# Optimization experiments

Hardware: AMD Instinct MI355X
Metric: run time of the kernel (lower is better)

The kernel has to match this reference:

```python
import jax, jax.numpy as jnp
import numpy as np

N, E, D_IN, D_HID, D_OUT = 100000, 1200000, 64, 64, 32


def setup_inputs() -> dict:
    key = jax.random.key(0)
    ks = jax.random.split(key, 8)
    x = jax.random.normal(ks[0], (N, D_IN), dtype=jnp.float32)
    edge_index = jax.random.randint(ks[1], (2, E), 0, N, dtype=jnp.int64)

    def w(k, din, dout):
        return jax.random.normal(k, (din, dout), dtype=jnp.float32) / jnp.sqrt(jnp.float32(din))

    return {
        "x": x,
        "edge_index": edge_index,
        # SAGEConv layer 1: lin_l (on aggregated neighbors, with bias) + lin_r (on self, no bias)
        "W_l1": w(ks[2], D_IN, D_HID),
        "W_r1": w(ks[3], D_IN, D_HID),
        "b1": jnp.zeros((D_HID,), jnp.float32),
        # SAGEConv layer 2
        "W_l2": w(ks[4], D_HID, D_OUT),
        "W_r2": w(ks[5], D_HID, D_OUT),
        "b2": jnp.zeros((D_OUT,), jnp.float32),
    }


def _sage_conv(x, src, dst, W_l, W_r, b, n_nodes):
    # mean-aggregate source features into destination nodes (PyG default 'mean')
    summed = jax.ops.segment_sum(x[src], dst, num_segments=n_nodes)          # [N, D]
    deg = jax.ops.segment_sum(jnp.ones(src.shape, x.dtype), dst, num_segments=n_nodes)
    mean = summed / jnp.maximum(deg, 1.0)[:, None]
    # out = lin_l(mean_neighbors) + lin_r(self)
    return mean @ W_l + b + x @ W_r


def reference(x, edge_index, W_l1, W_r1, b1, W_l2, W_r2, b2):
    src, dst = edge_index[0], edge_index[1]
    n_nodes = x.shape[0]
    h = _sage_conv(x, src, dst, W_l1, W_r1, b1, n_nodes)
    h = jax.nn.relu(h)
    out = _sage_conv(h, src, dst, W_l2, W_r2, b2, n_nodes)
    return out
```

## Files before the change

### kernel.cpp

```cpp
#include <hip/hip_runtime.h>
#include <hip/hip_bf16.h>


#define CHUNK 2048
#define BSHIFT 7
#define BCAP  2048

typedef __attribute__((ext_vector_type(8))) short bf8;
typedef __attribute__((ext_vector_type(4))) float f4;

__device__ __forceinline__ unsigned short f2b(float f) {
    unsigned u = __float_as_uint(f);
    u += 0x7FFF + ((u >> 16) & 1);
    return (unsigned short)(u >> 16);
}
__device__ __forceinline__ float blo(unsigned u) { return __uint_as_float(u << 16); }
__device__ __forceinline__ float bhi(unsigned u) { return __uint_as_float(u & 0xFFFF0000u); }

__device__ __forceinline__ bf8 load8f(const float* __restrict__ p) {
    float4 u0 = *(const float4*)p, u1 = *(const float4*)(p + 4);
    bf8 r;
    r[0] = (short)f2b(u0.x); r[1] = (short)f2b(u0.y);
    r[2] = (short)f2b(u0.z); r[3] = (short)f2b(u0.w);
    r[4] = (short)f2b(u1.x); r[5] = (short)f2b(u1.y);
    r[6] = (short)f2b(u1.z); r[7] = (short)f2b(u1.w);
    return r;
}

__device__ __forceinline__ int edge_src(const int* ei, int E, int e, bool i64) {
    return i64 ? ei[2 * e] : ei[e];
}
__device__ __forceinline__ int edge_dst(const int* ei, int E, int e, bool i64) {
    return i64 ? ei[2 * E + 2 * e] : ei[E + e];
}

__global__ __launch_bounds__(256) void mega1(
        const int* __restrict__ ei, int E, int* __restrict__ gcursor,
        int* __restrict__ bucketed, int nbuck, int nwg,
        const float* __restrict__ x,
        const float* __restrict__ Wl1, const float* __restrict__ Wr1,
        const float* __restrict__ b1,
        unsigned short* __restrict__ P1b, float* __restrict__ H, int n) {
    __shared__ int lhist[1024];
    __shared__ int wgbase[1024];
    __shared__ int sflag;
    int t = threadIdx.x;
    if ((int)blockIdx.x < nwg) {
        if (t == 0) sflag = 0;
#pragma unroll
        for (int i = 0; i < 4; ++i) lhist[t + 256 * i] = 0;
        __syncthreads();
        int base = blockIdx.x * CHUNK;
        int myor = 0;
#pragma unroll
        for (int i = 0; i < CHUNK / 256; ++i) {
            int e = base + i * 256 + t;
            if (e < E) myor |= ei[2 * e + 1];
        }
        if (myor) atomicOr(&sflag, 1);
        __syncthreads();
        bool i64 = (sflag == 0);
        int p[CHUNK / 256];
        int bk[CHUNK / 256];
#pragma unroll
        for (int i = 0; i < CHUNK / 256; ++i) {
            int e = base + i * 256 + t;
            if (e < E) {
                int s = edge_src(ei, E, e, i64);
                int d = edge_dst(ei, E, e, i64);
                p[i] = s | ((d & 127) << 24);
                bk[i] = d >> BSHIFT;
                atomicAdd(&lhist[bk[i]], 1);
            } else {
                bk[i] = -1;
            }
        }
        __syncthreads();
        for (int b = t; b < nbuck; b += 256) {
            int c = lhist[b];
            wgbase[b] = c ? atomicAdd(&gcursor[b], c) : 0;
            lhist[b] = 0;
        }
        __syncthreads();
#pragma unroll
        for (int i = 0; i < CHUNK / 256; ++i) {
            if (bk[i] >= 0) {
                int r = atomicAdd(&lhist[bk[i]], 1);
                int off = wgbase[bk[i]] + r;
                if (off < BCAP) bucketed[(size_t)bk[i] * BCAP + off] = p[i];
            }
        }
    } else {
        int mb = blockIdx.x - nwg;
        int lane = t & 63, w = t >> 6;
        int rb = mb * 64;
        int r15 = lane & 15, kg = lane >> 4;
        bf8 a[4][2];
#pragma unroll
        for (int rt = 0; rt < 4; ++rt) {
            int row = rb + rt * 16 + r15; if (row >= n) row = n - 1;
            const float* ap = x + (size_t)row * 64 + kg * 8;
            a[rt][0] = load8f(ap);
            a[rt][1] = load8f(ap + 32);
        }
        bf8 b[2][2];
#pragma unroll
        for (int ct2 = 0; ct2 < 2; ++ct2) {
            int c = (w * 2 + ct2) * 16 + r15;
#pragma unroll
            for (int ks = 0; ks < 2; ++ks) {
                bf8 bv;
#pragma unroll
                for (int j = 0; j < 8; ++j) {
                    int k = ks * 32 + kg * 8 + j;
                    float wv = (c < 64) ? Wl1[k * 64 + c] : Wr1[k * 64 + (c - 64)];
                    bv[j] = (short)f2b(wv);
                }
                b[ct2][ks] = bv;
            }
        }
        f4 acc[4][2] = {};
#pragma unroll
        for (int rt = 0; rt < 4; ++rt)
#pragma unroll
            for (int ct2 = 0; ct2 < 2; ++ct2)
#pragma unroll
                for (int ks = 0; ks < 2; ++ks)
                    acc[rt][ct2] = __builtin_amdgcn_mfma_f32_16x16x32_bf16(
                        a[rt][ks], b[ct2][ks], acc[rt][ct2], 0, 0, 0);
#pragma unroll
        for (int ct2 = 0; ct2 < 2; ++ct2) {
            int col = (w * 2 + ct2) * 16 + r15;
            bool isH = col >= 64;
            float bias = isH ? b1[col - 64] : 0.f;
#pragma unroll
            for (int rt = 0; rt < 4; ++rt) {
                int row0 = rb + rt * 16 + kg * 4;
#pragma unroll
                for (int reg = 0; reg < 4; ++reg) {
                    int row = row0 + reg;
                    if (row < n) {
                        float val = acc[rt][ct2][reg];
                        if (isH) H[(size_t)row * 64 + (col - 64)] = val + bias;
                        else     P1b[(size_t)row * 64 + col] = f2b(val);
                    }
                }
            }
        }
    }
}

__global__ __launch_bounds__(256) void k_bfinal(
        const int* __restrict__ bucketed, const int* __restrict__ gcursor,
        int* __restrict__ rs, int* __restrict__ re,
        int* __restrict__ adj, int n) {
    __shared__ int ledge[BCAP];
    __shared__ unsigned short lrank[BCAP];
    __shared__ int ldeg[128];
    __shared__ int lstart[257];
    int t = threadIdx.x, b = blockIdx.x;
    int start = b * BCAP;
    int cnt = gcursor[b];
    if (cnt > BCAP) cnt = BCAP;
    for (int i = t; i < cnt; i += 256) ledge[i] = bucketed[start + i];
    if (t < 128) ldeg[t] = 0;
    __syncthreads();
    for (int i = t; i < cnt; i += 256) {
        int dl = ((unsigned)ledge[i]) >> 24;
        lrank[i] = (unsigned short)atomicAdd(&ldeg[dl], 1);
    }
    __syncthreads();
    int v = (t < 128) ? ldeg[t] : 0;
    lstart[t + 1] = v;
    if (t == 0) lstart[0] = 0;
    __syncthreads();
    for (int off = 1; off < 256; off <<= 1) {
        int add = (t + 1 > off) ? lstart[t + 1 - off] : 0;
        __syncthreads();
        lstart[t + 1] += add;
        __syncthreads();
    }
    int node = b * 128 + t;
    if (t < 128 && node < n) {
        rs[node] = start + lstart[t];
        re[node] = start + lstart[t] + ldeg[t];
    }
    for (int i = t; i < cnt; i += 256) {
        int p = ledge[i];
        int dl = ((unsigned)p) >> 24;
        adj[start + lstart[dl] + lrank[i]] = p & 0xFFFFFF;
    }
}

__global__ __launch_bounds__(256) void agg1(
        const unsigned short* __restrict__ P1b, const int* __restrict__ rs,
        const int* __restrict__ re, const int* __restrict__ adj,
        const float* __restrict__ H, unsigned short* __restrict__ hb, int n) {
    int w = threadIdx.x >> 6, lane = threadIdx.x & 63;
    int v = blockIdx.x * 4 + w;
    if (v >= n) return;
    int s0 = rs[v], s1 = re[v], last = s1 - 1;
    int e8 = lane >> 3, f8 = lane & 7;
    float acc[8] = {0.f, 0.f, 0.f, 0.f, 0.f, 0.f, 0.f, 0.f};
    const uint4* P4 = (const uint4*)P1b;
    for (int e = s0; e < s1; e += 16) {
#pragma unroll
        for (int u = 0; u < 2; ++u) {
            int ei = e + u * 8 + e8;
            int ec = ei > last ? last : ei;
            int src = adj[ec];
            uint4 q = P4[(size_t)src * 8 + f8];
            float m = (ei <= last) ? 1.f : 0.f;
            acc[0] = fmaf(m, blo(q.x), acc[0]);
            acc[1] = fmaf(m, bhi(q.x), acc[1]);
            acc[2] = fmaf(m, blo(q.y), acc[2]);
            acc[3] = fmaf(m, bhi(q.y), acc[3]);
            acc[4] = fmaf(m, blo(q.z), acc[4]);
            acc[5] = fmaf(m, bhi(q.z), acc[5]);
            acc[6] = fmaf(m, blo(q.w), acc[6]);
            acc[7] = fmaf(m, bhi(q.w), acc[7]);
        }
    }
#pragma unroll
    for (int off = 8; off <= 32; off <<= 1)
#pragma unroll
        for (int i = 0; i < 8; ++i) acc[i] += __shfl_xor(acc[i], off);
    if (lane < 8) {
        float inv = 1.f / fmaxf((float)(s1 - s0), 1.f);
        const float4* H4 = (const float4*)(H + (size_t)v * 64);
        float4 ha = H4[lane * 2], hc = H4[lane * 2 + 1];
        float h0 = fmaxf(fmaf(acc[0], inv, ha.x), 0.f);
        float h1 = fmaxf(fmaf(acc[1], inv, ha.y), 0.f);
        float h2 = fmaxf(fmaf(acc[2], inv, ha.z), 0.f);
        float h3 = fmaxf(fmaf(acc[3], inv, ha.w), 0.f);
        float h4 = fmaxf(fmaf(acc[4], inv, hc.x), 0.f);
        float h5 = fmaxf(fmaf(acc[5], inv, hc.y), 0.f);
        float h6 = fmaxf(fmaf(acc[6], inv, hc.z), 0.f);
        float h7 = fmaxf(fmaf(acc[7], inv, hc.w), 0.f);
        uint4 o;
        o.x = f2b(h0) | ((unsigned)f2b(h1) << 16);
        o.y = f2b(h2) | ((unsigned)f2b(h3) << 16);
        o.z = f2b(h4) | ((unsigned)f2b(h5) << 16);
        o.w = f2b(h6) | ((unsigned)f2b(h7) << 16);
        ((uint4*)hb)[(size_t)v * 8 + lane] = o;
    }
}

__global__ __launch_bounds__(256) void mm2(
        const unsigned short* __restrict__ hb,
        const float* __restrict__ Wl2, const float* __restrict__ Wr2,
        const float* __restrict__ b2, unsigned short* __restrict__ zs, int n) {
    int lane = threadIdx.x & 63;
    int w = threadIdx.x >> 6;
    int rb = blockIdx.x * 64;
    int r15 = lane & 15, kg = lane >> 4;
    bf8 a[4][2];
#pragma unroll
    for (int rt = 0; rt < 4; ++rt) {
        int row = rb + rt * 16 + r15; if (row >= n) row = n - 1;
        const unsigned short* ap = hb + (size_t)row * 64 + kg * 8;
        a[rt][0] = *(const bf8*)(ap);
        a[rt][1] = *(const bf8*)(ap + 32);
    }
    int c = w * 16 + r15;
    bf8 b[2];
#pragma unroll
    for (int ks = 0; ks < 2; ++ks) {
        bf8 bv;
#pragma unroll
        for (int j = 0; j < 8; ++j) {
            int k = ks * 32 + kg * 8 + j;
            float wv = (c < 32) ? Wl2[k * 32 + c] : Wr2[k * 32 + (c - 32)];
            bv[j] = (short)f2b(wv);
        }
        b[ks] = bv;
    }
    f4 acc[4] = {};
#pragma unroll
    for (int rt = 0; rt < 4; ++rt)
#pragma unroll
        for (int ks = 0; ks < 2; ++ks)
            acc[rt] = __builtin_amdgcn_mfma_f32_16x16x32_bf16(
                a[rt][ks], b[ks], acc[rt], 0, 0, 0);
    bool isS = c >= 32;
    float bias = isS ? b2[c - 32] : 0.f;
#pragma unroll
    for (int rt = 0; rt < 4; ++rt) {
        int row0 = rb + rt * 16 + kg * 4;
#pragma unroll
        for (int reg = 0; reg < 4; ++reg) {
            int row = row0 + reg;
            if (row < n) zs[(size_t)row * 64 + c] = f2b(acc[rt][reg] + bias);
        }
    }
}

__global__ __launch_bounds__(256) void agg2(
        const unsigned short* __restrict__ zs, const int* __restrict__ rs,
        const int* __restrict__ re, const int* __restrict__ adj,
        float* __restrict__ out, int n) {
    int w = threadIdx.x >> 6, lane = threadIdx.x & 63;
    int v = blockIdx.x * 4 + w;
    if (v >= n) return;
    int s0 = rs[v], s1 = re[v], last = s1 - 1;
    int e16 = lane >> 2, f4c = lane & 3;
    float acc[8] = {0.f, 0.f, 0.f, 0.f, 0.f, 0.f, 0.f, 0.f};
    const uint4* Z4 = (const uint4*)zs;
    for (int e = s0; e < s1; e += 16) {
        int ei = e + e16;
        int ec = ei > last ? last : ei;
        int src = adj[ec];
        uint4 q = Z4[(size_t)src * 8 + f4c];
        float m = (ei <= last) ? 1.f : 0.f;
        acc[0] = fmaf(m, blo(q.x), acc[0]);
        acc[1] = fmaf(m, bhi(q.x), acc[1]);
        acc[2] = fmaf(m, blo(q.y), acc[2]);
        acc[3] = fmaf(m, bhi(q.y), acc[3]);
        acc[4] = fmaf(m, blo(q.z), acc[4]);
        acc[5] = fmaf(m, bhi(q.z), acc[5]);
        acc[6] = fmaf(m, blo(q.w), acc[6]);
        acc[7] = fmaf(m, bhi(q.w), acc[7]);
    }
#pragma unroll
    for (int off = 4; off <= 32; off <<= 1)
#pragma unroll
        for (int i = 0; i < 8; ++i) acc[i] += __shfl_xor(acc[i], off);
    if (lane < 4) {
        float inv = 1.f / fmaxf((float)(s1 - s0), 1.f);
        const uint4* srow = (const uint4*)(zs + (size_t)v * 64 + 32);
        uint4 u0 = srow[lane];
        float sv[8] = {blo(u0.x), bhi(u0.x), blo(u0.y), bhi(u0.y),
                       blo(u0.z), bhi(u0.z), blo(u0.w), bhi(u0.w)};
        float4 o0, o1;
        o0.x = fmaf(acc[0], inv, sv[0]);
        o0.y = fmaf(acc[1], inv, sv[1]);
        o0.z = fmaf(acc[2], inv, sv[2]);
        o0.w = fmaf(acc[3], inv, sv[3]);
        o1.x = fmaf(acc[4], inv, sv[4]);
        o1.y = fmaf(acc[5], inv, sv[5]);
        o1.z = fmaf(acc[6], inv, sv[6]);
        o1.w = fmaf(acc[7], inv, sv[7]);
        ((float4*)(out + (size_t)v * 32))[lane * 2] = o0;
        ((float4*)(out + (size_t)v * 32))[lane * 2 + 1] = o1;
    }
}

extern "C" void kernel_launch(void* const* d_in, const int* in_sizes, int n_in,
                              void* d_out, int out_size, void* d_ws, size_t ws_size,
                              hipStream_t stream) {
    const float* x   = (const float*)d_in[0];
    const int*   ei  = (const int*)d_in[1];
    const float* Wl1 = (const float*)d_in[2];
    const float* Wr1 = (const float*)d_in[3];
    const float* b1  = (const float*)d_in[4];
    const float* Wl2 = (const float*)d_in[5];
    const float* Wr2 = (const float*)d_in[6];
    const float* b2  = (const float*)d_in[7];

    int N = in_sizes[0] / 64;
    int E = in_sizes[1] / 2;
    int nbuck = (N + 127) >> BSHIFT;

    char* ws = (char*)d_ws;
    size_t o = 0;
    auto alloc = [&](size_t bytes) -> char* {
        char* p = ws + o;
        o = (o + bytes + 255) & ~(size_t)255;
        return p;
    };
    int* gcursor  = (int*)alloc((size_t)nbuck * 4);
    int* rs       = (int*)alloc((size_t)N * 4);
    int* re       = (int*)alloc((size_t)N * 4);
    int* bucketed = (int*)alloc((size_t)nbuck * BCAP * 4);
    unsigned short* P1b  = (unsigned short*)alloc((size_t)N * 64 * 2);
    unsigned short* hbuf = (unsigned short*)alloc((size_t)N * 64 * 2);
    float* H      = (float*)alloc((size_t)N * 64 * 4);
    int* adj = bucketed;
    unsigned short* zs = (unsigned short*)H;

    hipMemsetAsync(gcursor, 0, (size_t)nbuck * 4, stream);

    int nwg  = (E + CHUNK - 1) / CHUNK;
    int nb64 = (N + 63) / 64;
    int nb4  = (N + 3) / 4;
    mega1<<<nwg + nb64, 256, 0, stream>>>(ei, E, gcursor, bucketed, nbuck, nwg,
                                          x, Wl1, Wr1, b1, P1b, H, N);
    k_bfinal<<<nbuck, 256, 0, stream>>>(bucketed, gcursor, rs, re, adj, N);
    agg1<<<nb4, 256, 0, stream>>>(P1b, rs, re, adj, H, hbuf, N);
    mm2<<<nb64, 256, 0, stream>>>(hbuf, Wl2, Wr2, b2, zs, N);
    agg2<<<nb4, 256, 0, stream>>>(zs, rs, re, adj, (float*)d_out, N);
}
```

Measured before the change: 155.9 us.

## Fuse layer-1 aggregation with layer-2 matmul and store self term in bf16

Merges the agg1 and mm2 kernels into one. Each 64-node block aggregates neighbour features into a shared-memory tile and then runs the MFMA layer-2 matmul on it, so the hidden activations never round-trip through global memory. The self/bias term H is now stored as bf16 instead of fp32, halving its write and read traffic. The cost is that each block has only 4 waves, each handling 16 nodes serially, which reduces parallelism and latency hiding in the gather-heavy aggregation, and the extra bf16 rounding of H slightly lowers precision.

```diff
diff --git a/kernel.cpp b/kernel.cpp
--- a/kernel.cpp
+++ b/kernel.cpp
@@ -40,7 +40,7 @@
         const float* __restrict__ x,
         const float* __restrict__ Wl1, const float* __restrict__ Wr1,
         const float* __restrict__ b1,
-        unsigned short* __restrict__ P1b, float* __restrict__ H, int n) {
+        unsigned short* __restrict__ P1b, unsigned short* __restrict__ Hb, int n) {
     __shared__ int lhist[1024];
     __shared__ int wgbase[1024];
     __shared__ int sflag;
@@ -141,7 +141,7 @@
                     int row = row0 + reg;
                     if (row < n) {
                         float val = acc[rt][ct2][reg];
-                        if (isH) H[(size_t)row * 64 + (col - 64)] = val + bias;
+                        if (isH) Hb[(size_t)row * 64 + (col - 64)] = f2b(val + bias);
                         else     P1b[(size_t)row * 64 + col] = f2b(val);
                     }
                 }
@@ -192,76 +192,78 @@
     }
 }
 
-__global__ __launch_bounds__(256) void agg1(
+__global__ __launch_bounds__(256) void agg1mm2(
         const unsigned short* __restrict__ P1b, const int* __restrict__ rs,
         const int* __restrict__ re, const int* __restrict__ adj,
-        const float* __restrict__ H, unsigned short* __restrict__ hb, int n) {
-    int w = threadIdx.x >> 6, lane = threadIdx.x & 63;
-    int v = blockIdx.x * 4 + w;
-    if (v >= n) return;
-    int s0 = rs[v], s1 = re[v], last = s1 - 1;
-    int e8 = lane >> 3, f8 = lane & 7;
-    float acc[8] = {0.f, 0.f, 0.f, 0.f, 0.f, 0.f, 0.f, 0.f};
-    const uint4* P4 = (const uint4*)P1b;
-    for (int e = s0; e < s1; e += 16) {
-#pragma unroll
-        for (int u = 0; u < 2; ++u) {
-            int ei = e + u * 8 + e8;
-            int ec = ei > last ? last : ei;
-            int src = adj[ec];
-            uint4 q = P4[(size_t)src * 8 + f8];
-            float m = (ei <= last) ? 1.f : 0.f;
-            acc[0] = fmaf(m, blo(q.x), acc[0]);
-            acc[1] = fmaf(m, bhi(q.x), acc[1]);
-            acc[2] = fmaf(m, blo(q.y), acc[2]);
-            acc[3] = fmaf(m, bhi(q.y), acc[3]);
-            acc[4] = fmaf(m, blo(q.z), acc[4]);
-            acc[5] = fmaf(m, bhi(q.z), acc[5]);
-            acc[6] = fmaf(m, blo(q.w), acc[6]);
-            acc[7] = fmaf(m, bhi(q.w), acc[7]);
-        }
-    }
-#pragma unroll
-    for (int off = 8; off <= 32; off <<= 1)
-#pragma unroll
-        for (int i = 0; i < 8; ++i) acc[i] += __shfl_xor(acc[i], off);
-    if (lane < 8) {
-        float inv = 1.f / fmaxf((float)(s1 - s0), 1.f);
-        const float4* H4 = (const float4*)(H + (size_t)v * 64);
-        float4 ha = H4[lane * 2], hc = H4[lane * 2 + 1];
-        float h0 = fmaxf(fmaf(acc[0], inv, ha.x), 0.f);
-        float h1 = fmaxf(fmaf(acc[1], inv, ha.y), 0.f);
-        float h2 = fmaxf(fmaf(acc[2], inv, ha.z), 0.f);
-        float h3 = fmaxf(fmaf(acc[3], inv, ha.w), 0.f);
-        float h4 = fmaxf(fmaf(acc[4], inv, hc.x), 0.f);
-        float h5 = fmaxf(fmaf(acc[5], inv, hc.y), 0.f);
-        float h6 = fmaxf(fmaf(acc[6], inv, hc.z), 0.f);
-        float h7 = fmaxf(fmaf(acc[7], inv, hc.w), 0.f);
-        uint4 o;
-        o.x = f2b(h0) | ((unsigned)f2b(h1) << 16);
-        o.y = f2b(h2) | ((unsigned)f2b(h3) << 16);
-        o.z = f2b(h4) | ((unsigned)f2b(h5) << 16);
-        o.w = f2b(h6) | ((unsigned)f2b(h7) << 16);
-        ((uint4*)hb)[(size_t)v * 8 + lane] = o;
-    }
-}
-
-__global__ __launch_bounds__(256) void mm2(
-        const unsigned short* __restrict__ hb,
+        const unsigned short* __restrict__ Hb,
         const float* __restrict__ Wl2, const float* __restrict__ Wr2,
         const float* __restrict__ b2, unsigned short* __restrict__ zs, int n) {
-    int lane = threadIdx.x & 63;
-    int w = threadIdx.x >> 6;
-    int rb = blockIdx.x * 64;
+    __shared__ unsigned short hl[64][72];
+    int w = threadIdx.x >> 6, lane = threadIdx.x & 63;
+    int vbase = blockIdx.x * 64;
+    int e8 = lane >> 3, f8 = lane & 7;
+    const uint4* P4 = (const uint4*)P1b;
+    for (int i = 0; i < 16; ++i) {
+        int lr = w * 16 + i;
+        int v = vbase + lr;
+        if (v < n) {
+            int s0 = rs[v], s1 = re[v], last = s1 - 1;
+            float acc[8] = {0.f, 0.f, 0.f, 0.f, 0.f, 0.f, 0.f, 0.f};
+            for (int e = s0; e < s1; e += 16) {
+#pragma unroll
+                for (int u = 0; u < 2; ++u) {
+                    int ei = e + u * 8 + e8;
+                    int ec = ei > last ? last : ei;
+                    int src = adj[ec];
+                    uint4 q = P4[(size_t)src * 8 + f8];
+                    float m = (ei <= last) ? 1.f : 0.f;
+                    acc[0] = fmaf(m, blo(q.x), acc[0]);
+                    acc[1] = fmaf(m, bhi(q.x), acc[1]);
+                    acc[2] = fmaf(m, blo(q.y), acc[2]);
+                    acc[3] = fmaf(m, bhi(q.y), acc[3]);
+                    acc[4] = fmaf(m, blo(q.z), acc[4]);
+                    acc[5] = fmaf(m, bhi(q.z), acc[5]);
+                    acc[6] = fmaf(m, blo(q.w), acc[6]);
+                    acc[7] = fmaf(m, bhi(q.w), acc[7]);
+                }
+            }
+#pragma unroll
+            for (int off = 8; off <= 32; off <<= 1)
+#pragma unroll
+                for (int j = 0; j < 8; ++j) acc[j] += __shfl_xor(acc[j], off);
+            if (lane < 8) {
+                float inv = 1.f / fmaxf((float)(s1 - s0), 1.f);
+                uint4 u = ((const uint4*)(Hb + (size_t)v * 64))[lane];
+                float hv[8] = {blo(u.x), bhi(u.x), blo(u.y), bhi(u.y),
+                               blo(u.z), bhi(u.z), blo(u.w), bhi(u.w)};
+                uint4 o;
+                float g0 = fmaxf(fmaf(acc[0], inv, hv[0]), 0.f);
+                float g1 = fmaxf(fmaf(acc[1], inv, hv[1]), 0.f);
+                float g2 = fmaxf(fmaf(acc[2], inv, hv[2]), 0.f);
+                float g3 = fmaxf(fmaf(acc[3], inv, hv[3]), 0.f);
+                float g4 = fmaxf(fmaf(acc[4], inv, hv[4]), 0.f);
+                float g5 = fmaxf(fmaf(acc[5], inv, hv[5]), 0.f);
+                float g6 = fmaxf(fmaf(acc[6], inv, hv[6]), 0.f);
+                float g7 = fmaxf(fmaf(acc[7], inv, hv[7]), 0.f);
+                o.x = f2b(g0) | ((unsigned)f2b(g1) << 16);
+                o.y = f2b(g2) | ((unsigned)f2b(g3) << 16);
+                o.z = f2b(g4) | ((unsigned)f2b(g5) << 16);
+                o.w = f2b(g6) | ((unsigned)f2b(g7) << 16);
+                *(uint4*)&hl[lr][lane * 8] = o;
+            }
+        } else if (lane < 8) {
+            uint4 z = make_uint4(0, 0, 0, 0);
+            *(uint4*)&hl[lr][lane * 8] = z;
+        }
+    }
+    __syncthreads();
     int r15 = lane & 15, kg = lane >> 4;
     bf8 a[4][2];
 #pragma unroll
-    for (int rt = 0; rt < 4; ++rt) {
-        int row = rb + rt * 16 + r15; if (row >= n) row = n - 1;
-        const unsigned short* ap = hb + (size_t)row * 64 + kg * 8;
-        a[rt][0] = *(const bf8*)(ap);
-        a[rt][1] = *(const bf8*)(ap + 32);
-    }
+    for (int rt = 0; rt < 4; ++rt)
+#pragma unroll
+        for (int ks = 0; ks < 2; ++ks)
+            a[rt][ks] = *(const bf8*)&hl[rt * 16 + r15][ks * 32 + kg * 8];
     int c = w * 16 + r15;
     bf8 b[2];
 #pragma unroll
@@ -286,7 +288,7 @@
     float bias = isS ? b2[c - 32] : 0.f;
 #pragma unroll
     for (int rt = 0; rt < 4; ++rt) {
-        int row0 = rb + rt * 16 + kg * 4;
+        int row0 = vbase + rt * 16 + kg * 4;
 #pragma unroll
         for (int reg = 0; reg < 4; ++reg) {
             int row = row0 + reg;
@@ -372,11 +374,10 @@
     int* rs       = (int*)alloc((size_t)N * 4);
     int* re       = (int*)alloc((size_t)N * 4);
     int* bucketed = (int*)alloc((size_t)nbuck * BCAP * 4);
-    unsigned short* P1b  = (unsigned short*)alloc((size_t)N * 64 * 2);
-    unsigned short* hbuf = (unsigned short*)alloc((size_t)N * 64 * 2);
-    float* H      = (float*)alloc((size_t)N * 64 * 4);
+    unsigned short* P1b = (unsigned short*)alloc((size_t)N * 64 * 2);
+    unsigned short* Hb  = (unsigned short*)alloc((size_t)N * 64 * 2);
+    unsigned short* zs  = (unsigned short*)alloc((size_t)N * 64 * 2);
     int* adj = bucketed;
-    unsigned short* zs = (unsigned short*)H;
 
     hipMemsetAsync(gcursor, 0, (size_t)nbuck * 4, stream);
 
@@ -384,9 +385,8 @@
     int nb64 = (N + 63) / 64;
     int nb4  = (N + 3) / 4;
     mega1<<<nwg + nb64, 256, 0, stream>>>(ei, E, gcursor, bucketed, nbuck, nwg,
-                                          x, Wl1, Wr1, b1, P1b, H, N);
+                                          x, Wl1, Wr1, b1, P1b, Hb, N);
     k_bfinal<<<nbuck, 256, 0, stream>>>(bucketed, gcursor, rs, re, adj, N);
-    agg1<<<nb4, 256, 0, stream>>>(P1b, rs, re, adj, H, hbuf, N);
-    mm2<<<nb64, 256, 0, stream>>>(hbuf, Wl2, Wr2, b2, zs, N);
+    agg1mm2<<<nb64, 256, 0, stream>>>(P1b, rs, re, adj, Hb, Wl2, Wr2, b2, zs, N);
     agg2<<<nb4, 256, 0, stream>>>(zs, rs, re, adj, (float*)d_out, N);
 }
```

Measured after the change: 172.2 us. 10.4% more time.
